# Kernel tuning notes

Measured on AMD Instinct MI355X. Metric: run time of the kernel, lower is better.

## Reference

```python
import jax, jax.numpy as jnp
import numpy as np

C = 256
R = 16
CR = C // R  # 16

def setup_inputs() -> dict:
    key = jax.random.key(0)
    k_x, k_w1, k_b1, k_w2, k_b2 = jax.random.split(key, 5)
    x = jax.random.normal(k_x, (16, C, 128, 128), dtype=jnp.float32)
    # 1x1 conv weights stored as [out, in] matrices
    w1 = jax.random.normal(k_w1, (CR, C), dtype=jnp.float32) * (1.0 / np.sqrt(C))
    b1 = jax.random.normal(k_b1, (CR,), dtype=jnp.float32) * 0.01
    w2 = jax.random.normal(k_w2, (C, CR), dtype=jnp.float32) * (1.0 / np.sqrt(CR))
    b2 = jax.random.normal(k_b2, (C,), dtype=jnp.float32) * 0.01
    return {"x": x, "w1": w1, "b1": b1, "w2": w2, "b2": b2}

def reference(x, w1, b1, w2, b2):
    # global average pool over H,W -> [B, C]
    pooled = jnp.mean(x, axis=(2, 3))
    # fc1 (1x1 conv) + LeakyReLU(0.01)
    h = jnp.einsum('bc,rc->br', pooled, w1) + b1
    h = jnp.where(h >= 0, h, 0.01 * h)
    # fc2 (1x1 conv) + sigmoid gate
    s = jax.nn.sigmoid(jnp.einsum('br,cr->bc', h, w2) + b2)
    # broadcast channel scale
    return x * s[:, :, None, None]
```

## Files before the change

kernel.cpp:

```cpp
#include <hip/hip_runtime.h>
#include <math.h>

#define BATCH 16
#define CH    256
#define CRR   16
#define HWSZ  16384
#define NPLANES (BATCH * CH)

typedef float vfloat4 __attribute__((ext_vector_type(4)));

__global__ __launch_bounds__(256) void pool_kernel(const float* __restrict__ x,
                                                   float* __restrict__ pooled) {
    const int bc = blockIdx.x;
    const int t  = threadIdx.x;
    const vfloat4* plane = reinterpret_cast<const vfloat4*>(x + (size_t)bc * HWSZ);

    float sum = 0.0f;
#pragma unroll
    for (int k = 0; k < 16; ++k) {
        vfloat4 v = plane[k * 256 + t];
        sum += (v.x + v.y) + (v.z + v.w);
    }

#pragma unroll
    for (int off = 32; off > 0; off >>= 1)
        sum += __shfl_down(sum, off, 64);

    __shared__ float part[4];
    const int lane = t & 63;
    const int wid  = t >> 6;
    if (lane == 0) part[wid] = sum;
    __syncthreads();
    if (t == 0) {
        float tot = (part[0] + part[1]) + (part[2] + part[3]);
        pooled[bc] = tot * (1.0f / 16384.0f);
    }
}

__global__ __launch_bounds__(256) void scale_kernel(const float* __restrict__ x,
                                                    const float* __restrict__ pooled,
                                                    const float* __restrict__ w1,
                                                    const float* __restrict__ b1,
                                                    const float* __restrict__ w2,
                                                    const float* __restrict__ b2,
                                                    float* __restrict__ out) {
    const int bc = (NPLANES - 1) - blockIdx.x;
    const int t  = threadIdx.x;
    const int b  = bc >> 8;
    const int c  = bc & 255;

    __shared__ float p_lds[CH];
    __shared__ float h_lds[CRR];

    p_lds[t] = pooled[b * CH + t];
    __syncthreads();

    {
        const int r   = t >> 4;
        const int seg = t & 15;
        const float* wrow = w1 + r * CH + seg * 16;
        const float* pp   = p_lds + seg * 16;
        float ps = 0.0f;
#pragma unroll
        for (int j = 0; j < 16; ++j)
            ps += pp[j] * wrow[j];
#pragma unroll
        for (int m = 8; m > 0; m >>= 1)
            ps += __shfl_xor(ps, m, 64);
        if (seg == 0) {
            float h = ps + b1[r];
            h_lds[r] = (h >= 0.0f) ? h : 0.01f * h;
        }
    }
    __syncthreads();

    float z = b2[c];
    {
        const float* wcol = w2 + c * CRR;
#pragma unroll
        for (int r = 0; r < CRR; ++r)
            z += h_lds[r] * wcol[r];
    }
    const float sc = 1.0f / (1.0f + expf(-z));

    const vfloat4* xin = reinterpret_cast<const vfloat4*>(x + (size_t)bc * HWSZ);
    vfloat4*       o   = reinterpret_cast<vfloat4*>(out + (size_t)bc * HWSZ);
#pragma unroll
    for (int k = 0; k < 16; ++k) {
        vfloat4 v = xin[k * 256 + t];
        v *= sc;
        __builtin_nontemporal_store(v, &o[k * 256 + t]);
    }
}

extern "C" void kernel_launch(void* const* d_in, const int* in_sizes, int n_in,
                              void* d_out, int out_size, void* d_ws, size_t ws_size,
                              hipStream_t stream) {
    const float* x  = (const float*)d_in[0];
    const float* w1 = (const float*)d_in[1];
    const float* b1 = (const float*)d_in[2];
    const float* w2 = (const float*)d_in[3];
    const float* b2 = (const float*)d_in[4];
    float* out    = (float*)d_out;
    float* pooled = (float*)d_ws;

    pool_kernel<<<NPLANES, 256, 0, stream>>>(x, pooled);
    scale_kernel<<<NPLANES, 256, 0, stream>>>(x, pooled, w1, b1, w2, b2, out);
}
```

Measured before the change: 481.7 us.

## Fuse pool and scale into persistent kernel with per-batch counters

Replaces the separate pool and scale kernels with one persistent kernel of 512 blocks that walks planes in a software pipeline. Each block pools plane i, then scales plane i-1 once that batch's 256 channel means have been published through an atomic counter. The aim is to remove the kernel boundary and let the second read of a plane hit cache while the first pass is still running. The risks are spin-wait stalls when batches finish unevenly, a possible deadlock if not all 512 blocks are co-resident, and an extra init launch.

```diff
diff --git a/kernel.cpp b/kernel.cpp
--- a/kernel.cpp
+++ b/kernel.cpp
@@ -6,90 +6,118 @@
 #define CRR   16
 #define HWSZ  16384
 #define NPLANES (BATCH * CH)
+#define NBLK  512
+#define ITER  (NPLANES / NBLK)
 
 typedef float vfloat4 __attribute__((ext_vector_type(4)));
 
-__global__ __launch_bounds__(256) void pool_kernel(const float* __restrict__ x,
-                                                   float* __restrict__ pooled) {
-    const int bc = blockIdx.x;
-    const int t  = threadIdx.x;
-    const vfloat4* plane = reinterpret_cast<const vfloat4*>(x + (size_t)bc * HWSZ);
+__global__ void init_kernel(unsigned int* __restrict__ cnt) {
+    if (threadIdx.x < BATCH) cnt[threadIdx.x] = 0u;
+}
 
-    float sum = 0.0f;
-#pragma unroll
-    for (int k = 0; k < 16; ++k) {
-        vfloat4 v = plane[k * 256 + t];
-        sum += (v.x + v.y) + (v.z + v.w);
-    }
-
-#pragma unroll
-    for (int off = 32; off > 0; off >>= 1)
-        sum += __shfl_down(sum, off, 64);
+__global__ __launch_bounds__(256, 2)
+void se_persistent(const float* __restrict__ x,
+                   const float* __restrict__ w1,
+                   const float* __restrict__ b1,
+                   const float* __restrict__ w2,
+                   const float* __restrict__ b2,
+                   float* __restrict__ out,
+                   float* pooled,
+                   unsigned int* cnt) {
+    const int p = blockIdx.x;
+    const int t = threadIdx.x;
 
     __shared__ float part[4];
-    const int lane = t & 63;
-    const int wid  = t >> 6;
-    if (lane == 0) part[wid] = sum;
-    __syncthreads();
-    if (t == 0) {
-        float tot = (part[0] + part[1]) + (part[2] + part[3]);
-        pooled[bc] = tot * (1.0f / 16384.0f);
-    }
-}
-
-__global__ __launch_bounds__(256) void scale_kernel(const float* __restrict__ x,
-                                                    const float* __restrict__ pooled,
-                                                    const float* __restrict__ w1,
-                                                    const float* __restrict__ b1,
-                                                    const float* __restrict__ w2,
-                                                    const float* __restrict__ b2,
-                                                    float* __restrict__ out) {
-    const int bc = (NPLANES - 1) - blockIdx.x;
-    const int t  = threadIdx.x;
-    const int b  = bc >> 8;
-    const int c  = bc & 255;
-
     __shared__ float p_lds[CH];
     __shared__ float h_lds[CRR];
+    __shared__ float s_gate;
 
-    p_lds[t] = pooled[b * CH + t];
-    __syncthreads();
+    int prev_plane = -1;
 
-    {
-        const int r   = t >> 4;
-        const int seg = t & 15;
-        const float* wrow = w1 + r * CH + seg * 16;
-        const float* pp   = p_lds + seg * 16;
-        float ps = 0.0f;
+    for (int i = 0; i <= ITER; ++i) {
+        if (i < ITER) {
+            const int plane = i * NBLK + p;
+            const int b     = plane >> 8;
+            const vfloat4* pl = reinterpret_cast<const vfloat4*>(x + (size_t)plane * HWSZ);
+            float sum = 0.0f;
 #pragma unroll
-        for (int j = 0; j < 16; ++j)
-            ps += pp[j] * wrow[j];
+            for (int k = 0; k < 16; ++k) {
+                vfloat4 v = pl[k * 256 + t];
+                sum += (v.x + v.y) + (v.z + v.w);
+            }
 #pragma unroll
-        for (int m = 8; m > 0; m >>= 1)
-            ps += __shfl_xor(ps, m, 64);
-        if (seg == 0) {
-            float h = ps + b1[r];
-            h_lds[r] = (h >= 0.0f) ? h : 0.01f * h;
+            for (int off = 32; off > 0; off >>= 1)
+                sum += __shfl_down(sum, off, 64);
+            if ((t & 63) == 0) part[t >> 6] = sum;
+            __syncthreads();
+            if (t == 0) {
+                float tot = (part[0] + part[1]) + (part[2] + part[3]);
+                __hip_atomic_store(&pooled[plane], tot * (1.0f / 16384.0f),
+                                   __ATOMIC_RELEASE, __HIP_MEMORY_SCOPE_AGENT);
+                atomicAdd(&cnt[b], 1u);
+            }
+            __syncthreads();
         }
-    }
-    __syncthreads();
 
-    float z = b2[c];
-    {
-        const float* wcol = w2 + c * CRR;
+        if (prev_plane >= 0) {
+            const int plane = prev_plane;
+            const int b     = plane >> 8;
+            const int c     = plane & 255;
+
+            if (t == 0) {
+                while (__hip_atomic_load(&cnt[b], __ATOMIC_ACQUIRE,
+                                         __HIP_MEMORY_SCOPE_AGENT) < (unsigned)CH) {
+                    __builtin_amdgcn_s_sleep(2);
+                }
+            }
+            __syncthreads();
+
+            p_lds[t] = __hip_atomic_load(&pooled[b * CH + t], __ATOMIC_RELAXED,
+                                         __HIP_MEMORY_SCOPE_AGENT);
+            __syncthreads();
+
+            {
+                const int r   = t >> 4;
+                const int seg = t & 15;
+                const float* wrow = w1 + r * CH + seg * 16;
+                const float* pp   = p_lds + seg * 16;
+                float ps = 0.0f;
 #pragma unroll
-        for (int r = 0; r < CRR; ++r)
-            z += h_lds[r] * wcol[r];
-    }
-    const float sc = 1.0f / (1.0f + expf(-z));
+                for (int j = 0; j < 16; ++j)
+                    ps += pp[j] * wrow[j];
+#pragma unroll
+                for (int m = 8; m > 0; m >>= 1)
+                    ps += __shfl_xor(ps, m, 64);
+                if (seg == 0) {
+                    float h = ps + b1[r];
+                    h_lds[r] = (h >= 0.0f) ? h : 0.01f * h;
+                }
+            }
+            __syncthreads();
 
-    const vfloat4* xin = reinterpret_cast<const vfloat4*>(x + (size_t)bc * HWSZ);
-    vfloat4*       o   = reinterpret_cast<vfloat4*>(out + (size_t)bc * HWSZ);
+            if (t == 0) {
+                float z = b2[c];
+                const float* wcol = w2 + c * CRR;
 #pragma unroll
-    for (int k = 0; k < 16; ++k) {
-        vfloat4 v = xin[k * 256 + t];
-        v *= sc;
-        __builtin_nontemporal_store(v, &o[k * 256 + t]);
+                for (int r = 0; r < CRR; ++r)
+                    z += h_lds[r] * wcol[r];
+                s_gate = 1.0f / (1.0f + expf(-z));
+            }
+            __syncthreads();
+            const float sc = s_gate;
+
+            const vfloat4* xin = reinterpret_cast<const vfloat4*>(x + (size_t)plane * HWSZ);
+            vfloat4*       o   = reinterpret_cast<vfloat4*>(out + (size_t)plane * HWSZ);
+#pragma unroll
+            for (int k = 0; k < 16; ++k) {
+                vfloat4 v = xin[k * 256 + t];
+                v *= sc;
+                __builtin_nontemporal_store(v, &o[k * 256 + t]);
+            }
+            __syncthreads();
+        }
+
+        if (i < ITER) prev_plane = i * NBLK + p;
     }
 }
 
@@ -102,8 +130,10 @@
     const float* w2 = (const float*)d_in[3];
     const float* b2 = (const float*)d_in[4];
     float* out    = (float*)d_out;
-    float* pooled = (float*)d_ws;
 
-    pool_kernel<<<NPLANES, 256, 0, stream>>>(x, pooled);
-    scale_kernel<<<NPLANES, 256, 0, stream>>>(x, pooled, w1, b1, w2, b2, out);
+    float*        pooled = (float*)d_ws;
+    unsigned int* cnt    = (unsigned int*)(pooled + NPLANES);
+
+    init_kernel<<<1, 64, 0, stream>>>(cnt);
+    se_persistent<<<NBLK, 256, 0, stream>>>(x, w1, b1, w2, b2, out, pooled, cnt);
 }
```

Measured after the change: 715.1 us. +48.5%, slower.
